# Performance work log

Measured on AMD Instinct MI355X. Metric: run time of the kernel, lower is better.

## Reference

```python
import jax, jax.numpy as jnp
import numpy as np

N_NODES = 50000


def _add_self_loops(edge_index, num_nodes):
    loop = jnp.arange(num_nodes, dtype=edge_index.dtype)
    row = jnp.concatenate([edge_index[0], loop])
    col = jnp.concatenate([edge_index[1], loop])
    return row, col


def _gcn_norm(row, col, num_nodes):
    # deg computed on target index with unit edge weights (PyG gcn_norm)
    deg = jax.ops.segment_sum(jnp.ones_like(col, dtype=jnp.float32), col,
                              num_segments=num_nodes)
    dis = jnp.where(deg > 0, jax.lax.rsqrt(jnp.maximum(deg, 1.0)), 0.0)
    return dis[row] * dis[col]  # [E]


def _gcn_conv(x, W, b, row, col, norm, num_nodes):
    h = x @ W                                  # dense transform first (PyG order)
    msg = h[row] * norm[:, None]               # gather + normalize
    out = jax.ops.segment_sum(msg, col, num_segments=num_nodes)  # scatter-add
    return out + b


def setup_inputs() -> dict:
    key = jax.random.key(0)
    ks = jax.random.split(key, 10)
    E = 800000
    x = jax.random.normal(ks[0], (N_NODES, 29), dtype=jnp.float32)
    edge_index = jax.random.randint(ks[1], (2, E), 0, N_NODES, dtype=jnp.int64)

    def glorot(k, fan_in, fan_out):
        s = jnp.sqrt(2.0 / (fan_in + fan_out)).astype(jnp.float32)
        return jax.random.normal(k, (fan_in, fan_out), dtype=jnp.float32) * s

    return {
        "x": x, "edge_index": edge_index,
        "W1": glorot(ks[2], 29, 96),  "b1": jnp.zeros((96,), jnp.float32),
        "W2": glorot(ks[3], 96, 128), "b2": jnp.zeros((128,), jnp.float32),
        "W3": glorot(ks[4], 128, 64), "b3": jnp.zeros((64,), jnp.float32),
        "W4": glorot(ks[5], 64, 32),  "b4": jnp.zeros((32,), jnp.float32),
    }


def reference(x, edge_index, W1, b1, W2, b2, W3, b3, W4, b4):
    row, col = _add_self_loops(edge_index, N_NODES)
    norm = _gcn_norm(row, col, N_NODES)  # same graph -> same norm for all layers
    h = _gcn_conv(x, W1, b1, row, col, norm, N_NODES)
    h = jax.nn.relu(h)
    # dropout(p=0.4) is identity in eval mode
    h = _gcn_conv(h, W2, b2, row, col, norm, N_NODES)
    h = _gcn_conv(h, W3, b3, row, col, norm, N_NODES)
    h = _gcn_conv(h, W4, b4, row, col, norm, N_NODES)
    return h
```

## Files before the change

### kernel.cpp

```cpp
#include <hip/hip_runtime.h>


constexpr int NN  = 50000;
constexpr int CAP = 64;
constexpr int AGB = (NN * 8 + 255) / 256;
constexpr int C1B = (NN + 255) / 256;
constexpr int PREPB = (NN * 32 + 64 + 255) / 256;
constexpr int W34XB = 17;
constexpr int W234XB = 13;
constexpr int PXB = 256;

typedef unsigned short u16;
typedef int iv4 __attribute__((ext_vector_type(4)));

__global__ void place_x_kernel(const int* __restrict__ row, const int* __restrict__ col,
                               int* __restrict__ cnt, u16* __restrict__ ell, int E) {
    const int g  = blockIdx.x & 7;
    const int bi = blockIdx.x >> 3;
    const int n4 = E >> 2;
    const int slice = (n4 + PXB - 1) / PXB;
    const int i0 = bi * slice;
    int i1 = i0 + slice; if (i1 > n4) i1 = n4;
    const iv4* cv = (const iv4*)col;
    const iv4* rv = (const iv4*)row;
#define PLACE1(cc, rr) {                                                        \
        const int c_ = (cc);                                                    \
        if ((((c_ >> 6) & 7) == g) && (unsigned)c_ < (unsigned)NN) {            \
            const int r_ = (rr);                                                \
            if ((unsigned)r_ < (unsigned)NN) {                                  \
                const int pos = atomicAdd(&cnt[c_], 1);                         \
                if (pos < CAP) ell[c_ * CAP + pos] = (u16)r_;                   \
            }                                                                   \
        }                                                                       \
    }
    for (int i = i0 + threadIdx.x; i < i1; i += 256) {
        const iv4 c4 = cv[i];
        const iv4 r4 = rv[i];
        PLACE1(c4.x, r4.x);
        PLACE1(c4.y, r4.y);
        PLACE1(c4.z, r4.z);
        PLACE1(c4.w, r4.w);
    }
    if (bi == 0) {
        for (int e = (n4 << 2) + threadIdx.x; e < E; e += 256) {
            const int c = col[e];
            if (((c >> 6) & 7) != g || (unsigned)c >= (unsigned)NN) continue;
            const int r = row[e];
            if ((unsigned)r >= (unsigned)NN) continue;
            const int pos = atomicAdd(&cnt[c], 1);
            if (pos < CAP) ell[c * CAP + pos] = (u16)r;
        }
    }
#undef PLACE1
}

__global__ void prep_all_kernel(const int* __restrict__ cnt, u16* __restrict__ ell,
                                const float* __restrict__ x, float* __restrict__ dis,
                                float* __restrict__ Ba, float* __restrict__ Bb,
                                float* __restrict__ c1d,
                                const float* __restrict__ W3, const float* __restrict__ W4,
                                const float* __restrict__ b3,
                                float* __restrict__ W34, float* __restrict__ v1) {
    if (blockIdx.x >= PREPB) {
        const int wid = (blockIdx.x - PREPB) * 256 + threadIdx.x;
        if (wid < 4096) {
            const int r = wid >> 5, j = wid & 31;
            float a = 0.f;
#pragma unroll 8
            for (int k = 0; k < 64; ++k) a = fmaf(W3[r * 64 + k], W4[k * 32 + j], a);
            W34[wid] = a;
        } else if (wid < 4128) {
            const int j = wid - 4096;
            float a = 0.f;
#pragma unroll 8
            for (int k = 0; k < 64; ++k) a = fmaf(b3[k], W4[k * 32 + j], a);
            v1[j] = a;
        }
        return;
    }
    const int idx = blockIdx.x * blockDim.x + threadIdx.x;
    if (idx < NN * 32) {
        const int n = idx >> 5, f = idx & 31;
        int m = cnt[n]; if (m > CAP) m = CAP;
        const float d = rsqrtf((float)m + 1.0f);
        Ba[idx] = (f < 29) ? x[n * 29 + f] * d : 0.f;
        if (f == 31) dis[n] = d;
        if (f == 30) {
            int mp = (m + 7) & ~7; if (mp > CAP) mp = CAP;
            for (int k = m; k < mp; ++k) ell[n * CAP + k] = (u16)NN;
        }
    } else {
        const int i = idx - NN * 32;
        if (i < 32) { Ba[NN * 32 + i] = 0.f; Bb[NN * 32 + i] = 0.f; }
        else if (i == 32) dis[NN] = 0.f;
        else if (i == 33) c1d[NN] = 0.f;
    }
}

template<int MODE>
__device__ __forceinline__ void agg32_body(const float* __restrict__ hs,
                                           const int* __restrict__ cnt,
                                           const u16* __restrict__ ell,
                                           const float* __restrict__ dis,
                                           const float* __restrict__ c1,
                                           const float* __restrict__ c2,
                                           const float* __restrict__ v1,
                                           const float* __restrict__ v2,
                                           const float* __restrict__ bv,
                                           float* __restrict__ out) {
    const int idx = blockIdx.x * blockDim.x + threadIdx.x;
    if (idx >= NN * 8) return;
    const int n = idx >> 3, c = idx & 7;
    const float4* hpc = (const float4*)hs + c;
    float4 acc = hpc[n * 8];
    int m = cnt[n]; if (m > CAP) m = CAP;
    const int m8 = (m + 7) >> 3;
    const int4* ip = (const int4*)(ell + (size_t)n * CAP);
    int t = 0;
    for (; t + 2 <= m8; t += 2) {
        const int4 sA = ip[t], sB = ip[t + 1];
        const unsigned ax = (unsigned)sA.x, ay = (unsigned)sA.y;
        const unsigned az = (unsigned)sA.z, aw = (unsigned)sA.w;
        const unsigned bx = (unsigned)sB.x, by = (unsigned)sB.y;
        const unsigned bz = (unsigned)sB.z, bw = (unsigned)sB.w;
        const float4 g0 = hpc[(ax & 0xFFFFu) * 8], g1 = hpc[(ax >> 16) * 8];
        const float4 g2 = hpc[(ay & 0xFFFFu) * 8], g3 = hpc[(ay >> 16) * 8];
        const float4 g4 = hpc[(az & 0xFFFFu) * 8], g5 = hpc[(az >> 16) * 8];
        const float4 g6 = hpc[(aw & 0xFFFFu) * 8], g7 = hpc[(aw >> 16) * 8];
        const float4 h0 = hpc[(bx & 0xFFFFu) * 8], h1 = hpc[(bx >> 16) * 8];
        const float4 h2 = hpc[(by & 0xFFFFu) * 8], h3 = hpc[(by >> 16) * 8];
        const float4 h4 = hpc[(bz & 0xFFFFu) * 8], h5 = hpc[(bz >> 16) * 8];
        const float4 h6 = hpc[(bw & 0xFFFFu) * 8], h7 = hpc[(bw >> 16) * 8];
        acc.x += (((g0.x + g1.x) + (g2.x + g3.x)) + ((g4.x + g5.x) + (g6.x + g7.x)))
               + (((h0.x + h1.x) + (h2.x + h3.x)) + ((h4.x + h5.x) + (h6.x + h7.x)));
        acc.y += (((g0.y + g1.y) + (g2.y + g3.y)) + ((g4.y + g5.y) + (g6.y + g7.y)))
               + (((h0.y + h1.y) + (h2.y + h3.y)) + ((h4.y + h5.y) + (h6.y + h7.y)));
        acc.z += (((g0.z + g1.z) + (g2.z + g3.z)) + ((g4.z + g5.z) + (g6.z + g7.z)))
               + (((h0.z + h1.z) + (h2.z + h3.z)) + ((h4.z + h5.z) + (h6.z + h7.z)));
        acc.w += (((g0.w + g1.w) + (g2.w + g3.w)) + ((g4.w + g5.w) + (g6.w + g7.w)))
               + (((h0.w + h1.w) + (h2.w + h3.w)) + ((h4.w + h5.w) + (h6.w + h7.w)));
    }
    if (t < m8) {
        const int4 s = ip[t];
        const unsigned ux = (unsigned)s.x, uy = (unsigned)s.y;
        const unsigned uz = (unsigned)s.z, uw = (unsigned)s.w;
        const float4 g0 = hpc[(ux & 0xFFFFu) * 8], g1 = hpc[(ux >> 16) * 8];
        const float4 g2 = hpc[(uy & 0xFFFFu) * 8], g3 = hpc[(uy >> 16) * 8];
        const float4 g4 = hpc[(uz & 0xFFFFu) * 8], g5 = hpc[(uz >> 16) * 8];
        const float4 g6 = hpc[(uw & 0xFFFFu) * 8], g7 = hpc[(uw >> 16) * 8];
        acc.x += ((g0.x + g1.x) + (g2.x + g3.x)) + ((g4.x + g5.x) + (g6.x + g7.x));
        acc.y += ((g0.y + g1.y) + (g2.y + g3.y)) + ((g4.y + g5.y) + (g6.y + g7.y));
        acc.z += ((g0.z + g1.z) + (g2.z + g3.z)) + ((g4.z + g5.z) + (g6.z + g7.z));
        acc.w += ((g0.w + g1.w) + (g2.w + g3.w)) + ((g4.w + g5.w) + (g6.w + g7.w));
    }
    const float d = dis[n];
    float4 r;
    if (MODE == 0) {
        r.x = acc.x * d; r.y = acc.y * d; r.z = acc.z * d; r.w = acc.w * d;
    } else if (MODE == 1) {
        const float d2 = d * d;
        r.x = acc.x * d2; r.y = acc.y * d2; r.z = acc.z * d2; r.w = acc.w * d2;
    } else {
        const float a1 = c1[n], a2 = c2[n];
        const float4 w1 = ((const float4*)v1)[c];
        const float4 w2 = ((const float4*)v2)[c];
        const float4 bb = ((const float4*)bv)[c];
        r.x = fmaf(acc.x, d, fmaf(a1, w1.x, fmaf(a2, w2.x, bb.x)));
        r.y = fmaf(acc.y, d, fmaf(a1, w1.y, fmaf(a2, w2.y, bb.y)));
        r.z = fmaf(acc.z, d, fmaf(a1, w1.z, fmaf(a2, w2.z, bb.z)));
        r.w = fmaf(acc.w, d, fmaf(a1, w1.w, fmaf(a2, w2.w, bb.w)));
    }
    ((float4*)out)[idx] = r;
}

__device__ __forceinline__ void agg1_body(const float* __restrict__ in,
                                          const int* __restrict__ cnt,
                                          const u16* __restrict__ ell,
                                          const float* __restrict__ dis,
                                          float* __restrict__ out,
                                          float* __restrict__ outd, int blk0) {
    const int n = (blockIdx.x - blk0) * 256 + threadIdx.x;
    if (n >= NN) return;
    float acc = in[n];
    int m = cnt[n]; if (m > CAP) m = CAP;
    const int m8 = (m + 7) >> 3;
    const int4* ip = (const int4*)(ell + (size_t)n * CAP);
    for (int t = 0; t < m8; ++t) {
        const int4 s = ip[t];
        const unsigned ux = (unsigned)s.x, uy = (unsigned)s.y;
        const unsigned uz = (unsigned)s.z, uw = (unsigned)s.w;
        acc += ((in[ux & 0xFFFFu] + in[ux >> 16]) + (in[uy & 0xFFFFu] + in[uy >> 16]))
             + ((in[uz & 0xFFFFu] + in[uz >> 16]) + (in[uw & 0xFFFFu] + in[uw >> 16]));
    }
    const float r = dis[n] * acc;
    out[n] = r;
    if (outd) outd[n] = r * dis[n];
}

__global__ void agg_pre_kernel(const float* __restrict__ Ba, const int* __restrict__ cnt,
                               const u16* __restrict__ ell, const float* __restrict__ dis,
                               float* __restrict__ Bb, float* __restrict__ c1,
                               float* __restrict__ c1d,
                               const float* __restrict__ W2, const float* __restrict__ b2,
                               const float* __restrict__ W34, float* __restrict__ W234,
                               float* __restrict__ v2) {
    if (blockIdx.x < AGB) {
        agg32_body<0>(Ba, cnt, ell, dis, nullptr, nullptr, nullptr, nullptr, nullptr, Bb);
    } else if (blockIdx.x < AGB + C1B) {
        agg1_body(dis, cnt, ell, dis, c1, c1d, AGB);
    } else {
        const int wid = (blockIdx.x - AGB - C1B) * 256 + threadIdx.x;
        if (wid < 3072) {
            const int r = wid >> 5, j = wid & 31;
            float a = 0.f;
#pragma unroll 8
            for (int k = 0; k < 128; ++k) a = fmaf(W2[r * 128 + k], W34[k * 32 + j], a);
            W234[wid] = a;
        } else if (wid < 3104) {
            const int j = wid - 3072;
            float a = 0.f;
#pragma unroll 8
            for (int k = 0; k < 128; ++k) a = fmaf(b2[k], W34[k * 32 + j], a);
            v2[j] = a;
        }
    }
}

__global__ void agg_hop1_kernel(const float* __restrict__ Ba, const int* __restrict__ cnt,
                                const u16* __restrict__ ell, const float* __restrict__ dis,
                                float* __restrict__ Bb, const float* __restrict__ c1d,
                                float* __restrict__ c2) {
    if (blockIdx.x < AGB)
        agg32_body<1>(Ba, cnt, ell, dis, nullptr, nullptr, nullptr, nullptr, nullptr, Bb);
    else
        agg1_body(c1d, cnt, ell, dis, c2, nullptr, AGB);
}

__global__ void agg_hop2_kernel(const float* __restrict__ Bb, const int* __restrict__ cnt,
                                const u16* __restrict__ ell, const float* __restrict__ dis,
                                float* __restrict__ Ba) {
    agg32_body<1>(Bb, cnt, ell, dis, nullptr, nullptr, nullptr, nullptr, nullptr, Ba);
}

__global__ void agg_hop3_kernel(const float* __restrict__ Ba, const int* __restrict__ cnt,
                                const u16* __restrict__ ell, const float* __restrict__ dis,
                                const float* __restrict__ c1, const float* __restrict__ c2,
                                const float* __restrict__ v1, const float* __restrict__ v2,
                                const float* __restrict__ bv, float* __restrict__ out) {
    agg32_body<2>(Ba, cnt, ell, dis, c1, c2, v1, v2, bv, out);
}

__global__ void __launch_bounds__(192, 2)
gemm_fused_kernel(const float* __restrict__ X, const float* __restrict__ W1,
                  const float* __restrict__ b1, const float* __restrict__ dis,
                  const float* __restrict__ W234, float* __restrict__ G) {
    constexpr int NPB = 16, RSX = 36, RSH = 104;
    __shared__ float xs[NPB * RSX];
    __shared__ float hsm[NPB * RSH];
    const int tid = threadIdx.x;
    const int n0  = blockIdx.x * NPB;

    const float4* Xv = (const float4*)(X + (size_t)n0 * 32);
    for (int i = tid; i < NPB * 8; i += 192) {
        const int nl = i >> 3, r = i & 7;
        float4 v = make_float4(0.f, 0.f, 0.f, 0.f);
        if (n0 + nl < NN) v = Xv[nl * 8 + r];
        *(float4*)(xs + nl * RSX + r * 4) = v;
    }
    __syncthreads();

    {
        const int cg = tid % 24, g = tid / 24;
        const float* x0 = xs + (2 * g) * RSX;
        const float* x1 = x0 + RSX;
        const float4* Wv = (const float4*)W1;
        float4 a0 = make_float4(0.f, 0.f, 0.f, 0.f);
        float4 a1 = make_float4(0.f, 0.f, 0.f, 0.f);
#pragma unroll
        for (int k = 0; k < 29; ++k) {
            const float4 w = Wv[k * 24 + cg];
            const float v0 = x0[k], v1 = x1[k];
            a0.x = fmaf(v0, w.x, a0.x); a0.y = fmaf(v0, w.y, a0.y);
            a0.z = fmaf(v0, w.z, a0.z); a0.w = fmaf(v0, w.w, a0.w);
            a1.x = fmaf(v1, w.x, a1.x); a1.y = fmaf(v1, w.y, a1.y);
            a1.z = fmaf(v1, w.z, a1.z); a1.w = fmaf(v1, w.w, a1.w);
        }
        const float4 bb = ((const float4*)b1)[cg];
#pragma unroll
        for (int h = 0; h < 2; ++h) {
            const int nl = 2 * g + h, node = n0 + nl;
            const float d = (node < NN) ? dis[node] : 0.f;
            const float4 a = h ? a1 : a0;
            float4 r;
            r.x = fmaxf(a.x + bb.x, 0.f) * d; r.y = fmaxf(a.y + bb.y, 0.f) * d;
            r.z = fmaxf(a.z + bb.z, 0.f) * d; r.w = fmaxf(a.w + bb.w, 0.f) * d;
            *(float4*)(hsm + nl * RSH + cg * 4) = r;
        }
    }
    __syncthreads();

    if (tid < 128) {
        const int nl = tid >> 3, cg = tid & 7;
        const float* hr = hsm + nl * RSH;
        const float4* Wv = (const float4*)W234;
        float4 a = make_float4(0.f, 0.f, 0.f, 0.f);
#pragma unroll 8
        for (int k = 0; k < 96; ++k) {
            const float4 w = Wv[k * 8 + cg];
            const float v = hr[k];
            a.x = fmaf(v, w.x, a.x); a.y = fmaf(v, w.y, a.y);
            a.z = fmaf(v, w.z, a.z); a.w = fmaf(v, w.w, a.w);
        }
        const int node = n0 + nl;
        if (node < NN) ((float4*)(G + (size_t)node * 32))[cg] = a;
    }
}

extern "C" void kernel_launch(void* const* d_in, const int* in_sizes, int n_in,
                              void* d_out, int out_size, void* d_ws, size_t ws_size,
                              hipStream_t stream) {
    const float* x  = (const float*)d_in[0];
    const int*   ei = (const int*)d_in[1];
    const float* W1 = (const float*)d_in[2]; const float* b1 = (const float*)d_in[3];
    const float* W2 = (const float*)d_in[4]; const float* b2 = (const float*)d_in[5];
    const float* W3 = (const float*)d_in[6]; const float* b3 = (const float*)d_in[7];
    const float* W4 = (const float*)d_in[8]; const float* b4p = (const float*)d_in[9];
    float* outp = (float*)d_out;

    const int E = in_sizes[1] / 2;
    const int* row = ei;
    const int* col = ei + E;

    int*   cnt  = (int*)d_ws;
    float* dis  = (float*)(cnt + 50048);
    u16*   ell  = (u16*)(dis + 50056);
    float* c1   = (float*)((int*)ell + 1600000);
    float* c1d  = c1 + 50056;
    float* c2   = c1d + 50056;
    float* W34  = c2 + 50056;
    float* W234 = W34 + 4096;
    float* v1   = W234 + 3072;
    float* v2   = v1 + 32;
    float* Ba   = v2 + 32;
    float* Bb   = Ba + 1600064;

    hipMemsetAsync(cnt, 0, 50048 * sizeof(int), stream);
    place_x_kernel<<<8 * PXB, 256, 0, stream>>>(row, col, cnt, ell, E);
    prep_all_kernel<<<PREPB + W34XB, 256, 0, stream>>>(cnt, ell, x, dis, Ba, Bb, c1d,
                                                       W3, W4, b3, W34, v1);
    agg_pre_kernel<<<AGB + C1B + W234XB, 256, 0, stream>>>(Ba, cnt, ell, dis, Bb, c1, c1d,
                                                           W2, b2, W34, W234, v2);
    gemm_fused_kernel<<<(NN + 15) / 16, 192, 0, stream>>>(Bb, W1, b1, dis, W234, Ba);
    agg_hop1_kernel<<<AGB + C1B, 256, 0, stream>>>(Ba, cnt, ell, dis, Bb, c1d, c2);
    agg_hop2_kernel<<<AGB, 256, 0, stream>>>(Bb, cnt, ell, dis, Ba);
    agg_hop3_kernel<<<AGB, 256, 0, stream>>>(Ba, cnt, ell, dis, c1, c2, v1, v2, b4p, outp);
}
```

Before: 223.5 us.

## Partition neighbor lists by source half and map each half to separate XCDs

Edges are split into two ELL structures by whether the source row lies in the lower or upper half of nodes. Each aggregation hop is done as two half-side partial sums, with blocks mapped so that XCDs 0-3 handle one half and XCDs 4-7 the other, so each XCD's L2 holds only half of the feature table. Separate combine kernels then add the partials and apply the normalisation. This adds extra kernels and extra partial-buffer traffic. The per-half cap of 32 could also drop edges for nodes with skewed in-degree.

```diff
diff --git a/kernel.cpp b/kernel.cpp
--- a/kernel.cpp
+++ b/kernel.cpp
@@ -1,20 +1,25 @@
 #include <hip/hip_runtime.h>
 
 
-constexpr int NN  = 50000;
-constexpr int CAP = 64;
-constexpr int AGB = (NN * 8 + 255) / 256;
-constexpr int C1B = (NN + 255) / 256;
+constexpr int NN   = 50000;
+constexpr int HALF = 25000;
+constexpr int CAPH = 32;
+constexpr int NCH  = 1564;
+constexpr int SBLK = NCH * 2;
+constexpr int CMB  = (NN * 8 + 255) / 256;
+constexpr int C1B  = (NN + 255) / 256;
 constexpr int PREPB = (NN * 32 + 64 + 255) / 256;
 constexpr int W34XB = 17;
 constexpr int W234XB = 13;
 constexpr int PXB = 256;
 
 typedef unsigned short u16;
-typedef int iv4 __attribute__((ext_vector_type(4)));
+typedef int   iv4 __attribute__((ext_vector_type(4)));
+typedef float fv4 __attribute__((ext_vector_type(4)));
 
 __global__ void place_x_kernel(const int* __restrict__ row, const int* __restrict__ col,
-                               int* __restrict__ cnt, u16* __restrict__ ell, int E) {
+                               int* __restrict__ cntA, int* __restrict__ cntB,
+                               u16* __restrict__ ellA, u16* __restrict__ ellB, int E) {
     const int g  = blockIdx.x & 7;
     const int bi = blockIdx.x >> 3;
     const int n4 = E >> 2;
@@ -28,8 +33,10 @@
         if ((((c_ >> 6) & 7) == g) && (unsigned)c_ < (unsigned)NN) {            \
             const int r_ = (rr);                                                \
             if ((unsigned)r_ < (unsigned)NN) {                                  \
-                const int pos = atomicAdd(&cnt[c_], 1);                         \
-                if (pos < CAP) ell[c_ * CAP + pos] = (u16)r_;                   \
+                int* cp  = (r_ < HALF) ? cntA : cntB;                           \
+                u16* ep  = (r_ < HALF) ? ellA : ellB;                           \
+                const int pos = atomicAdd(&cp[c_], 1);                          \
+                if (pos < CAPH) ep[c_ * CAPH + pos] = (u16)r_;                  \
             }                                                                   \
         }                                                                       \
     }
@@ -47,14 +54,17 @@
             if (((c >> 6) & 7) != g || (unsigned)c >= (unsigned)NN) continue;
             const int r = row[e];
             if ((unsigned)r >= (unsigned)NN) continue;
-            const int pos = atomicAdd(&cnt[c], 1);
-            if (pos < CAP) ell[c * CAP + pos] = (u16)r;
+            int* cp = (r < HALF) ? cntA : cntB;
+            u16* ep = (r < HALF) ? ellA : ellB;
+            const int pos = atomicAdd(&cp[c], 1);
+            if (pos < CAPH) ep[c * CAPH + pos] = (u16)r;
         }
     }
 #undef PLACE1
 }
 
-__global__ void prep_all_kernel(const int* __restrict__ cnt, u16* __restrict__ ell,
+__global__ void prep_all_kernel(const int* __restrict__ cntA, const int* __restrict__ cntB,
+                                u16* __restrict__ ellA, u16* __restrict__ ellB,
                                 const float* __restrict__ x, float* __restrict__ dis,
                                 float* __restrict__ Ba, float* __restrict__ Bb,
                                 float* __restrict__ c1d,
@@ -81,13 +91,18 @@
     const int idx = blockIdx.x * blockDim.x + threadIdx.x;
     if (idx < NN * 32) {
         const int n = idx >> 5, f = idx & 31;
-        int m = cnt[n]; if (m > CAP) m = CAP;
-        const float d = rsqrtf((float)m + 1.0f);
+        int mA = cntA[n]; if (mA > CAPH) mA = CAPH;
+        int mB = cntB[n]; if (mB > CAPH) mB = CAPH;
+        const float d = rsqrtf((float)(mA + mB) + 1.0f);
         Ba[idx] = (f < 29) ? x[n * 29 + f] * d : 0.f;
         if (f == 31) dis[n] = d;
         if (f == 30) {
-            int mp = (m + 7) & ~7; if (mp > CAP) mp = CAP;
-            for (int k = m; k < mp; ++k) ell[n * CAP + k] = (u16)NN;
+            int mp = (mA + 7) & ~7; if (mp > CAPH) mp = CAPH;
+            for (int k = mA; k < mp; ++k) ellA[n * CAPH + k] = (u16)NN;
+        }
+        if (f == 29) {
+            int mp = (mB + 7) & ~7; if (mp > CAPH) mp = CAPH;
+            for (int k = mB; k < mp; ++k) ellB[n * CAPH + k] = (u16)NN;
         }
     } else {
         const int i = idx - NN * 32;
@@ -97,51 +112,31 @@
     }
 }
 
-template<int MODE>
-__device__ __forceinline__ void agg32_body(const float* __restrict__ hs,
-                                           const int* __restrict__ cnt,
-                                           const u16* __restrict__ ell,
-                                           const float* __restrict__ dis,
-                                           const float* __restrict__ c1,
-                                           const float* __restrict__ c2,
-                                           const float* __restrict__ v1,
-                                           const float* __restrict__ v2,
-                                           const float* __restrict__ bv,
-                                           float* __restrict__ out) {
-    const int idx = blockIdx.x * blockDim.x + threadIdx.x;
-    if (idx >= NN * 8) return;
-    const int n = idx >> 3, c = idx & 7;
-    const float4* hpc = (const float4*)hs + c;
-    float4 acc = hpc[n * 8];
-    int m = cnt[n]; if (m > CAP) m = CAP;
-    const int m8 = (m + 7) >> 3;
-    const int4* ip = (const int4*)(ell + (size_t)n * CAP);
-    int t = 0;
-    for (; t + 2 <= m8; t += 2) {
-        const int4 sA = ip[t], sB = ip[t + 1];
-        const unsigned ax = (unsigned)sA.x, ay = (unsigned)sA.y;
-        const unsigned az = (unsigned)sA.z, aw = (unsigned)sA.w;
-        const unsigned bx = (unsigned)sB.x, by = (unsigned)sB.y;
-        const unsigned bz = (unsigned)sB.z, bw = (unsigned)sB.w;
-        const float4 g0 = hpc[(ax & 0xFFFFu) * 8], g1 = hpc[(ax >> 16) * 8];
-        const float4 g2 = hpc[(ay & 0xFFFFu) * 8], g3 = hpc[(ay >> 16) * 8];
-        const float4 g4 = hpc[(az & 0xFFFFu) * 8], g5 = hpc[(az >> 16) * 8];
-        const float4 g6 = hpc[(aw & 0xFFFFu) * 8], g7 = hpc[(aw >> 16) * 8];
-        const float4 h0 = hpc[(bx & 0xFFFFu) * 8], h1 = hpc[(bx >> 16) * 8];
-        const float4 h2 = hpc[(by & 0xFFFFu) * 8], h3 = hpc[(by >> 16) * 8];
-        const float4 h4 = hpc[(bz & 0xFFFFu) * 8], h5 = hpc[(bz >> 16) * 8];
-        const float4 h6 = hpc[(bw & 0xFFFFu) * 8], h7 = hpc[(bw >> 16) * 8];
-        acc.x += (((g0.x + g1.x) + (g2.x + g3.x)) + ((g4.x + g5.x) + (g6.x + g7.x)))
-               + (((h0.x + h1.x) + (h2.x + h3.x)) + ((h4.x + h5.x) + (h6.x + h7.x)));
-        acc.y += (((g0.y + g1.y) + (g2.y + g3.y)) + ((g4.y + g5.y) + (g6.y + g7.y)))
-               + (((h0.y + h1.y) + (h2.y + h3.y)) + ((h4.y + h5.y) + (h6.y + h7.y)));
-        acc.z += (((g0.z + g1.z) + (g2.z + g3.z)) + ((g4.z + g5.z) + (g6.z + g7.z)))
-               + (((h0.z + h1.z) + (h2.z + h3.z)) + ((h4.z + h5.z) + (h6.z + h7.z)));
-        acc.w += (((g0.w + g1.w) + (g2.w + g3.w)) + ((g4.w + g5.w) + (g6.w + g7.w)))
-               + (((h0.w + h1.w) + (h2.w + h3.w)) + ((h4.w + h5.w) + (h6.w + h7.w)));
-    }
-    if (t < m8) {
-        const int4 s = ip[t];
+__device__ __forceinline__ void side_body(const float* __restrict__ h,
+                                          const int* __restrict__ cntA,
+                                          const int* __restrict__ cntB,
+                                          const u16* __restrict__ ellA,
+                                          const u16* __restrict__ ellB,
+                                          float* __restrict__ Pa,
+                                          float* __restrict__ Pb) {
+    const int bid  = blockIdx.x;
+    const int xcd  = bid & 7;
+    const int side = xcd >> 2;
+    const int sub  = (bid >> 3) * 4 + (xcd & 3);
+    const int n    = sub * 32 + (threadIdx.x >> 3);
+    if (n >= NN) return;
+    const int c = threadIdx.x & 7;
+    const int*  cntS = side ? cntB : cntA;
+    const u16*  ellS = side ? ellB : ellA;
+    float*      P    = side ? Pb : Pa;
+    const float4* hpc = (const float4*)h + c;
+    const bool selfme = side ? (n >= HALF) : (n < HALF);
+    float4 acc = selfme ? hpc[n * 8] : make_float4(0.f, 0.f, 0.f, 0.f);
+    int m = cntS[n]; if (m > CAPH) m = CAPH;
+    const int q = (m + 7) >> 3;
+    const iv4* ip = (const iv4*)(ellS + (size_t)n * CAPH);
+    for (int t = 0; t < q; ++t) {
+        const iv4 s = __builtin_nontemporal_load(ip + t);
         const unsigned ux = (unsigned)s.x, uy = (unsigned)s.y;
         const unsigned uz = (unsigned)s.z, uw = (unsigned)s.w;
         const float4 g0 = hpc[(ux & 0xFFFFu) * 8], g1 = hpc[(ux >> 16) * 8];
@@ -153,63 +148,56 @@
         acc.z += ((g0.z + g1.z) + (g2.z + g3.z)) + ((g4.z + g5.z) + (g6.z + g7.z));
         acc.w += ((g0.w + g1.w) + (g2.w + g3.w)) + ((g4.w + g5.w) + (g6.w + g7.w));
     }
-    const float d = dis[n];
-    float4 r;
-    if (MODE == 0) {
-        r.x = acc.x * d; r.y = acc.y * d; r.z = acc.z * d; r.w = acc.w * d;
-    } else if (MODE == 1) {
-        const float d2 = d * d;
-        r.x = acc.x * d2; r.y = acc.y * d2; r.z = acc.z * d2; r.w = acc.w * d2;
-    } else {
-        const float a1 = c1[n], a2 = c2[n];
-        const float4 w1 = ((const float4*)v1)[c];
-        const float4 w2 = ((const float4*)v2)[c];
-        const float4 bb = ((const float4*)bv)[c];
-        r.x = fmaf(acc.x, d, fmaf(a1, w1.x, fmaf(a2, w2.x, bb.x)));
-        r.y = fmaf(acc.y, d, fmaf(a1, w1.y, fmaf(a2, w2.y, bb.y)));
-        r.z = fmaf(acc.z, d, fmaf(a1, w1.z, fmaf(a2, w2.z, bb.z)));
-        r.w = fmaf(acc.w, d, fmaf(a1, w1.w, fmaf(a2, w2.w, bb.w)));
-    }
-    ((float4*)out)[idx] = r;
+    fv4 r; r.x = acc.x; r.y = acc.y; r.z = acc.z; r.w = acc.w;
+    __builtin_nontemporal_store(r, (fv4*)P + (size_t)n * 8 + c);
 }
 
 __device__ __forceinline__ void agg1_body(const float* __restrict__ in,
-                                          const int* __restrict__ cnt,
-                                          const u16* __restrict__ ell,
+                                          const int* __restrict__ cntA,
+                                          const int* __restrict__ cntB,
+                                          const u16* __restrict__ ellA,
+                                          const u16* __restrict__ ellB,
                                           const float* __restrict__ dis,
                                           float* __restrict__ out,
                                           float* __restrict__ outd, int blk0) {
     const int n = (blockIdx.x - blk0) * 256 + threadIdx.x;
     if (n >= NN) return;
     float acc = in[n];
-    int m = cnt[n]; if (m > CAP) m = CAP;
-    const int m8 = (m + 7) >> 3;
-    const int4* ip = (const int4*)(ell + (size_t)n * CAP);
-    for (int t = 0; t < m8; ++t) {
-        const int4 s = ip[t];
-        const unsigned ux = (unsigned)s.x, uy = (unsigned)s.y;
-        const unsigned uz = (unsigned)s.z, uw = (unsigned)s.w;
-        acc += ((in[ux & 0xFFFFu] + in[ux >> 16]) + (in[uy & 0xFFFFu] + in[uy >> 16]))
-             + ((in[uz & 0xFFFFu] + in[uz >> 16]) + (in[uw & 0xFFFFu] + in[uw >> 16]));
+#pragma unroll
+    for (int s = 0; s < 2; ++s) {
+        const int* cntS = s ? cntB : cntA;
+        const u16* ellS = s ? ellB : ellA;
+        int m = cntS[n]; if (m > CAPH) m = CAPH;
+        const int q = (m + 7) >> 3;
+        const iv4* ip = (const iv4*)(ellS + (size_t)n * CAPH);
+        for (int t = 0; t < q; ++t) {
+            const iv4 v = ip[t];
+            const unsigned ux = (unsigned)v.x, uy = (unsigned)v.y;
+            const unsigned uz = (unsigned)v.z, uw = (unsigned)v.w;
+            acc += ((in[ux & 0xFFFFu] + in[ux >> 16]) + (in[uy & 0xFFFFu] + in[uy >> 16]))
+                 + ((in[uz & 0xFFFFu] + in[uz >> 16]) + (in[uw & 0xFFFFu] + in[uw >> 16]));
+        }
     }
     const float r = dis[n] * acc;
     out[n] = r;
     if (outd) outd[n] = r * dis[n];
 }
 
-__global__ void agg_pre_kernel(const float* __restrict__ Ba, const int* __restrict__ cnt,
-                               const u16* __restrict__ ell, const float* __restrict__ dis,
-                               float* __restrict__ Bb, float* __restrict__ c1,
-                               float* __restrict__ c1d,
+__global__ void agg_pre_kernel(const float* __restrict__ Ba,
+                               const int* __restrict__ cntA, const int* __restrict__ cntB,
+                               const u16* __restrict__ ellA, const u16* __restrict__ ellB,
+                               const float* __restrict__ dis,
+                               float* __restrict__ Pa, float* __restrict__ Pb,
+                               float* __restrict__ c1, float* __restrict__ c1d,
                                const float* __restrict__ W2, const float* __restrict__ b2,
                                const float* __restrict__ W34, float* __restrict__ W234,
                                float* __restrict__ v2) {
-    if (blockIdx.x < AGB) {
-        agg32_body<0>(Ba, cnt, ell, dis, nullptr, nullptr, nullptr, nullptr, nullptr, Bb);
-    } else if (blockIdx.x < AGB + C1B) {
-        agg1_body(dis, cnt, ell, dis, c1, c1d, AGB);
+    if (blockIdx.x < SBLK) {
+        side_body(Ba, cntA, cntB, ellA, ellB, Pa, Pb);
+    } else if (blockIdx.x < SBLK + C1B) {
+        agg1_body(dis, cntA, cntB, ellA, ellB, dis, c1, c1d, SBLK);
     } else {
-        const int wid = (blockIdx.x - AGB - C1B) * 256 + threadIdx.x;
+        const int wid = (blockIdx.x - SBLK - C1B) * 256 + threadIdx.x;
         if (wid < 3072) {
             const int r = wid >> 5, j = wid & 31;
             float a = 0.f;
@@ -226,33 +214,67 @@
     }
 }
 
-__global__ void agg_hop1_kernel(const float* __restrict__ Ba, const int* __restrict__ cnt,
-                                const u16* __restrict__ ell, const float* __restrict__ dis,
-                                float* __restrict__ Bb, const float* __restrict__ c1d,
-                                float* __restrict__ c2) {
-    if (blockIdx.x < AGB)
-        agg32_body<1>(Ba, cnt, ell, dis, nullptr, nullptr, nullptr, nullptr, nullptr, Bb);
+__global__ void agg_hop1_kernel(const float* __restrict__ h,
+                                const int* __restrict__ cntA, const int* __restrict__ cntB,
+                                const u16* __restrict__ ellA, const u16* __restrict__ ellB,
+                                const float* __restrict__ dis,
+                                float* __restrict__ Pa, float* __restrict__ Pb,
+                                const float* __restrict__ c1d, float* __restrict__ c2) {
+    if (blockIdx.x < SBLK)
+        side_body(h, cntA, cntB, ellA, ellB, Pa, Pb);
     else
-        agg1_body(c1d, cnt, ell, dis, c2, nullptr, AGB);
-}
-
-__global__ void agg_hop2_kernel(const float* __restrict__ Bb, const int* __restrict__ cnt,
-                                const u16* __restrict__ ell, const float* __restrict__ dis,
-                                float* __restrict__ Ba) {
-    agg32_body<1>(Bb, cnt, ell, dis, nullptr, nullptr, nullptr, nullptr, nullptr, Ba);
-}
-
-__global__ void agg_hop3_kernel(const float* __restrict__ Ba, const int* __restrict__ cnt,
-                                const u16* __restrict__ ell, const float* __restrict__ dis,
-                                const float* __restrict__ c1, const float* __restrict__ c2,
-                                const float* __restrict__ v1, const float* __restrict__ v2,
-                                const float* __restrict__ bv, float* __restrict__ out) {
-    agg32_body<2>(Ba, cnt, ell, dis, c1, c2, v1, v2, bv, out);
+        agg1_body(c1d, cntA, cntB, ellA, ellB, dis, c2, nullptr, SBLK);
+}
+
+__global__ void agg_side_kernel(const float* __restrict__ h,
+                                const int* __restrict__ cntA, const int* __restrict__ cntB,
+                                const u16* __restrict__ ellA, const u16* __restrict__ ellB,
+                                float* __restrict__ Pa, float* __restrict__ Pb) {
+    side_body(h, cntA, cntB, ellA, ellB, Pa, Pb);
+}
+
+__global__ void comb_kernel(const float* __restrict__ Pa, const float* __restrict__ Pb,
+                            const float* __restrict__ dis, float* __restrict__ out) {
+    const int idx = blockIdx.x * 256 + threadIdx.x;
+    if (idx >= NN * 8) return;
+    const int n = idx >> 3;
+    const float d = dis[n];
+    const float d2 = d * d;
+    const float4 a = ((const float4*)Pa)[idx];
+    const float4 b = ((const float4*)Pb)[idx];
+    float4 r;
+    r.x = (a.x + b.x) * d2; r.y = (a.y + b.y) * d2;
+    r.z = (a.z + b.z) * d2; r.w = (a.w + b.w) * d2;
+    ((float4*)out)[idx] = r;
+}
+
+__global__ void final_kernel(const float* __restrict__ Pa, const float* __restrict__ Pb,
+                             const float* __restrict__ dis,
+                             const float* __restrict__ c1, const float* __restrict__ c2,
+                             const float* __restrict__ v1, const float* __restrict__ v2,
+                             const float* __restrict__ bv, float* __restrict__ out) {
+    const int idx = blockIdx.x * 256 + threadIdx.x;
+    if (idx >= NN * 8) return;
+    const int n = idx >> 3, c = idx & 7;
+    const float d = dis[n];
+    const float4 a = ((const float4*)Pa)[idx];
+    const float4 b = ((const float4*)Pb)[idx];
+    const float a1 = c1[n], a2 = c2[n];
+    const float4 w1 = ((const float4*)v1)[c];
+    const float4 w2 = ((const float4*)v2)[c];
+    const float4 bb = ((const float4*)bv)[c];
+    float4 r;
+    r.x = fmaf(a.x + b.x, d, fmaf(a1, w1.x, fmaf(a2, w2.x, bb.x)));
+    r.y = fmaf(a.y + b.y, d, fmaf(a1, w1.y, fmaf(a2, w2.y, bb.y)));
+    r.z = fmaf(a.z + b.z, d, fmaf(a1, w1.z, fmaf(a2, w2.z, bb.z)));
+    r.w = fmaf(a.w + b.w, d, fmaf(a1, w1.w, fmaf(a2, w2.w, bb.w)));
+    ((float4*)out)[idx] = r;
 }
 
 __global__ void __launch_bounds__(192, 2)
-gemm_fused_kernel(const float* __restrict__ X, const float* __restrict__ W1,
-                  const float* __restrict__ b1, const float* __restrict__ dis,
+gemm_fused_kernel(const float* __restrict__ Pa, const float* __restrict__ Pb,
+                  const float* __restrict__ W1, const float* __restrict__ b1,
+                  const float* __restrict__ dis,
                   const float* __restrict__ W234, float* __restrict__ G) {
     constexpr int NPB = 16, RSX = 36, RSH = 104;
     __shared__ float xs[NPB * RSX];
@@ -260,11 +282,17 @@
     const int tid = threadIdx.x;
     const int n0  = blockIdx.x * NPB;
 
-    const float4* Xv = (const float4*)(X + (size_t)n0 * 32);
     for (int i = tid; i < NPB * 8; i += 192) {
         const int nl = i >> 3, r = i & 7;
+        const int node = n0 + nl;
         float4 v = make_float4(0.f, 0.f, 0.f, 0.f);
-        if (n0 + nl < NN) v = Xv[nl * 8 + r];
+        if (node < NN) {
+            const float d = dis[node];
+            const float4 a = ((const float4*)Pa)[(size_t)node * 8 + r];
+            const float4 b = ((const float4*)Pb)[(size_t)node * 8 + r];
+            v.x = (a.x + b.x) * d; v.y = (a.y + b.y) * d;
+            v.z = (a.z + b.z) * d; v.w = (a.w + b.w) * d;
+        }
         *(float4*)(xs + nl * RSX + r * 4) = v;
     }
     __syncthreads();
@@ -331,10 +359,12 @@
     const int* row = ei;
     const int* col = ei + E;
 
-    int*   cnt  = (int*)d_ws;
-    float* dis  = (float*)(cnt + 50048);
-    u16*   ell  = (u16*)(dis + 50056);
-    float* c1   = (float*)((int*)ell + 1600000);
+    int*   cntA = (int*)d_ws;
+    int*   cntB = cntA + 50048;
+    float* dis  = (float*)(cntB + 50048);
+    u16*   ellA = (u16*)(dis + 50056);
+    u16*   ellB = (u16*)((int*)ellA + 800768);
+    float* c1   = (float*)((int*)ellB + 800768);
     float* c1d  = c1 + 50056;
     float* c2   = c1d + 50056;
     float* W34  = c2 + 50056;
@@ -343,15 +373,22 @@
     float* v2   = v1 + 32;
     float* Ba   = v2 + 32;
     float* Bb   = Ba + 1600064;
-
-    hipMemsetAsync(cnt, 0, 50048 * sizeof(int), stream);
-    place_x_kernel<<<8 * PXB, 256, 0, stream>>>(row, col, cnt, ell, E);
-    prep_all_kernel<<<PREPB + W34XB, 256, 0, stream>>>(cnt, ell, x, dis, Ba, Bb, c1d,
-                                                       W3, W4, b3, W34, v1);
-    agg_pre_kernel<<<AGB + C1B + W234XB, 256, 0, stream>>>(Ba, cnt, ell, dis, Bb, c1, c1d,
-                                                           W2, b2, W34, W234, v2);
-    gemm_fused_kernel<<<(NN + 15) / 16, 192, 0, stream>>>(Bb, W1, b1, dis, W234, Ba);
-    agg_hop1_kernel<<<AGB + C1B, 256, 0, stream>>>(Ba, cnt, ell, dis, Bb, c1d, c2);
-    agg_hop2_kernel<<<AGB, 256, 0, stream>>>(Bb, cnt, ell, dis, Ba);
-    agg_hop3_kernel<<<AGB, 256, 0, stream>>>(Ba, cnt, ell, dis, c1, c2, v1, v2, b4p, outp);
-}
+    float* Pa   = Bb + 1600064;
+    float* Pb   = Pa + 1600064;
+
+    hipMemsetAsync(cntA, 0, 2 * 50048 * sizeof(int), stream);
+    place_x_kernel<<<8 * PXB, 256, 0, stream>>>(row, col, cntA, cntB, ellA, ellB, E);
+    prep_all_kernel<<<PREPB + W34XB, 256, 0, stream>>>(cntA, cntB, ellA, ellB, x, dis,
+                                                       Ba, Bb, c1d, W3, W4, b3, W34, v1);
+    agg_pre_kernel<<<SBLK + C1B + W234XB, 256, 0, stream>>>(Ba, cntA, cntB, ellA, ellB,
+                                                            dis, Pa, Pb, c1, c1d,
+                                                            W2, b2, W34, W234, v2);
+    gemm_fused_kernel<<<(NN + 15) / 16, 192, 0, stream>>>(Pa, Pb, W1, b1, dis, W234, Ba);
+    agg_hop1_kernel<<<SBLK + C1B, 256, 0, stream>>>(Ba, cntA, cntB, ellA, ellB, dis,
+                                                    Pa, Pb, c1d, c2);
+    comb_kernel<<<CMB, 256, 0, stream>>>(Pa, Pb, dis, Bb);
+    agg_side_kernel<<<SBLK, 256, 0, stream>>>(Bb, cntA, cntB, ellA, ellB, Pa, Pb);
+    comb_kernel<<<CMB, 256, 0, stream>>>(Pa, Pb, dis, Ba);
+    agg_side_kernel<<<SBLK, 256, 0, stream>>>(Ba, cntA, cntB, ellA, ellB, Pa, Pb);
+    final_kernel<<<CMB, 256, 0, stream>>>(Pa, Pb, dis, c1, c2, v1, v2, b4p, outp);
+}
```

Measured after the change: 248.5 us. 1.11x slower.
